# Kernel tuning notes

Measured on AMD Instinct MI355X. Metric: run time of the kernel, lower is better.

Reference implementation:

```python
import jax, jax.numpy as jnp
import numpy as np

D_MODEL = 1024
N_HEADS = 16
DK = D_MODEL // N_HEADS


def setup_inputs() -> dict:
    key = jax.random.key(0)
    k1, k2, k3, k4 = jax.random.split(key, 4)
    x = jax.random.normal(k1, (2, 2048, D_MODEL), dtype=jnp.float32)
    # torch nn.Linear stores weight as [out_features, in_features]
    W_qkv = jax.random.normal(k2, (3 * D_MODEL, D_MODEL), dtype=jnp.float32) * (1.0 / np.sqrt(D_MODEL))
    W_proj = jax.random.normal(k3, (D_MODEL, D_MODEL), dtype=jnp.float32) * (1.0 / np.sqrt(D_MODEL))
    b_proj = jax.random.normal(k4, (D_MODEL,), dtype=jnp.float32) * 0.01
    return {"x": x, "W_qkv": W_qkv, "W_proj": W_proj, "b_proj": b_proj}


def reference(x, W_qkv, W_proj, b_proj):
    B, L, D = x.shape
    qkv = x @ W_qkv.T                      # [B, L, 3D]
    q, k, v = jnp.split(qkv, 3, axis=-1)   # each [B, L, D]

    def split_heads(t):
        return t.reshape(B, L, N_HEADS, DK).transpose(0, 2, 1, 3)  # [B, H, L, dk]

    q, k, v = map(split_heads, (q, k, v))
    scale = jnp.float32(1.0 / np.sqrt(DK))
    scores = jnp.einsum('bhid,bhjd->bhij', q, k) * scale  # [B, H, L, L]
    attn = jax.nn.softmax(scores, axis=-1)
    out = jnp.einsum('bhij,bhjd->bhid', attn, v)           # [B, H, L, dk]
    out = out.transpose(0, 2, 1, 3).reshape(B, L, D)
    return out @ W_proj.T + b_proj
```

## Files before the change

kernel.cpp:

```cpp
#include <hip/hip_runtime.h>
#include <stdint.h>

typedef unsigned short ushort_t;
typedef __bf16 bf16x4 __attribute__((ext_vector_type(4)));
typedef __bf16 bf16x8 __attribute__((ext_vector_type(8)));
typedef float f32x4 __attribute__((ext_vector_type(4)));
typedef float f32x16 __attribute__((ext_vector_type(16)));
typedef unsigned short us8 __attribute__((ext_vector_type(8)));
typedef unsigned short us4v __attribute__((ext_vector_type(4)));

__device__ __forceinline__ float bf2f(ushort_t u) {
  union { uint32_t u; float f; } v; v.u = ((uint32_t)u) << 16; return v.f;
}
__device__ __forceinline__ ushort_t f2bf(float f) {
  union { float f; uint32_t u; } v; v.f = f;
  uint32_t u = v.u;
  uint32_t r = (u + 0x7FFFu + ((u >> 16) & 1u)) >> 16;
  return (ushort_t)r;
}
__device__ __forceinline__ uint32_t pkbf(float a, float b) {
  __bf16 x = (__bf16)a, y = (__bf16)b;
  uint32_t ux = __builtin_bit_cast(unsigned short, x);
  uint32_t uy = __builtin_bit_cast(unsigned short, y);
  return ux | (uy << 16);
}
__device__ __forceinline__ void gload_lds16(const void* g, void* l) {
  __builtin_amdgcn_global_load_lds(
      (const __attribute__((address_space(1))) void*)g,
      (__attribute__((address_space(3))) void*)l, 16, 0, 0);
}
__device__ __forceinline__ void tr2(const ushort_t* p, bf16x4& lo, bf16x4& hi) {
  asm volatile("ds_read_b64_tr_b16 %0, %2\n\t"
               "ds_read_b64_tr_b16 %1, %2 offset:128"
               : "=&v"(lo), "=&v"(hi)
               : "v"((const __attribute__((address_space(3))) ushort_t*)p));
}

template <typename T> __device__ __forceinline__ T to_out(float f);
template <> __device__ __forceinline__ ushort_t to_out<ushort_t>(float f) { return f2bf(f); }
template <> __device__ __forceinline__ float to_out<float>(float f) { return f; }

#define SCQ 0.1803368801111204f

__global__ void f2b3_kernel(const float* __restrict__ a, ushort_t* __restrict__ ao,
                            const float* __restrict__ b, ushort_t* __restrict__ bo,
                            const float* __restrict__ c, ushort_t* __restrict__ co) {
  int blk = blockIdx.x;
  const float* src; ushort_t* dst; int n4, b0, nb;
  if (blk < 1024)      { src = a; dst = ao; n4 = 1048576; b0 = blk;        nb = 1024; }
  else if (blk < 1792) { src = b; dst = bo; n4 = 786432;  b0 = blk - 1024; nb = 768; }
  else                 { src = c; dst = co; n4 = 262144;  b0 = blk - 1792; nb = 256; }
  for (int i = b0 * 256 + threadIdx.x; i < n4; i += nb * 256) {
    float4 v = ((const float4*)src)[i];
    us4v o;
    o[0] = f2bf(v.x); o[1] = f2bf(v.y); o[2] = f2bf(v.z); o[3] = f2bf(v.w);
    ((us4v*)dst)[i] = o;
  }
}

template<bool BIAS, typename OT, bool SCALEQ>
__global__ __launch_bounds__(256, 2) void gemm_bt(
    const ushort_t* __restrict__ A, const ushort_t* __restrict__ W,
    const float* __restrict__ bias, OT* __restrict__ C,
    int M, int N, int K)
{
  __shared__ ushort_t As[128 * 64];
  __shared__ ushort_t Bs[128 * 64];
  const int t = threadIdx.x;
  const int w = t >> 6, lane = t & 63;
  const int lg = lane >> 4, lc = lane & 15;

  const int NX = N >> 7;
  const int nwg = gridDim.x;
  const int o = blockIdx.x;
  const int id = (o & 7) * (nwg >> 3) + (o >> 3);
  const int rowbase = (id / NX) * 128;
  const int colbase = (id % NX) * 128;
  const int wr = (w >> 1) * 64, wc = (w & 1) * 64;

  f32x4 acc[4][4] = {};
  const int nkt = K >> 6;

  for (int kt = 0; kt < nkt; ++kt) {
#pragma unroll
    for (int i = 0; i < 4; ++i) {
      int off = (i * 256 + t) * 16;
      int row = off >> 7;
      int cb  = off & 127;
      int ec  = cb ^ ((row & 7) << 4);
      gload_lds16(A + (size_t)(rowbase + row) * K + kt * 64 + (ec >> 1),
                  (char*)As + off);
      gload_lds16(W + (size_t)(colbase + row) * K + kt * 64 + (ec >> 1),
                  (char*)Bs + off);
    }
    __syncthreads();
#pragma unroll
    for (int kk = 0; kk < 2; ++kk) {
      bf16x8 af[4], bf[4];
#pragma unroll
      for (int m = 0; m < 4; ++m) {
        int row = wr + m * 16 + lc;
        int kb  = (lg * 16 + kk * 64) ^ ((row & 7) << 4);
        af[m] = *(const bf16x8*)((const char*)As + row * 128 + kb);
        int col = wc + m * 16 + lc;
        int kb2 = (lg * 16 + kk * 64) ^ ((col & 7) << 4);
        bf[m] = *(const bf16x8*)((const char*)Bs + col * 128 + kb2);
      }
#pragma unroll
      for (int m = 0; m < 4; ++m)
#pragma unroll
        for (int n = 0; n < 4; ++n)
          acc[m][n] = __builtin_amdgcn_mfma_f32_16x16x32_bf16(af[m], bf[n],
                                                              acc[m][n], 0, 0, 0);
    }
    __syncthreads();
  }

#pragma unroll
  for (int m = 0; m < 4; ++m) {
    int r0 = rowbase + wr + m * 16 + lg * 4;
#pragma unroll
    for (int n = 0; n < 4; ++n) {
      int c0 = colbase + wc + n * 16 + lc;
      float bv = 0.f;
      if (BIAS) bv = bias[c0];
      float qs = 1.f;
      if (SCALEQ) qs = (c0 < 1024) ? SCQ : 1.f;
#pragma unroll
      for (int j = 0; j < 4; ++j)
        C[(size_t)(r0 + j) * N + c0] = to_out<OT>(acc[m][n][j] * qs + bv);
    }
  }
}

__global__ __launch_bounds__(512, 4) void attn_fwd(
    const ushort_t* __restrict__ qkv, ushort_t* __restrict__ o1,
    ushort_t* __restrict__ o2, float* __restrict__ lbuf)
{
  __shared__ ushort_t Ks[2][64 * 64];
  __shared__ ushort_t Vs[2][64 * 64];

  const int t = threadIdx.x, w = t >> 6, lane = t & 63;
  const int l31 = lane & 31, hi = lane >> 5;
  const int lc = lane & 15;

  const int d = blockIdx.x;
  const int qt = (d >> 3) & 7;
  const int bhs = (d & 7) * 8 + (d >> 6);
  const int bh = bhs >> 1, split = bhs & 1;
  const int b = bh >> 4, h = bh & 15;

  const ushort_t* Qg = qkv + (size_t)(b * 2048) * 3072 + h * 64;
  const ushort_t* Kg = Qg + 1024 + (size_t)split * 1024 * 3072;
  const ushort_t* Vg = Qg + 2048 + (size_t)split * 1024 * 3072;

  auto stage_k = [&](ushort_t* Kd, int kt) {
    int off = t * 16;
    int row = off >> 7;
    int cb  = off & 127;
    int ec  = cb ^ ((row & 7) << 4);
    gload_lds16(Kg + (size_t)(kt * 64 + row) * 3072 + (ec >> 1),
                (char*)Kd + off);
  };
  const int vr  = t >> 3;
  const int vc0 = (t & 7) * 8;
  const int vdst = (vc0 >> 4) * 2048 + (vr >> 2) * 128 + (vr & 3) * 32 +
                   (vc0 & 8) * 2;

  const ushort_t* qrow_p = Qg + (size_t)(qt * 256 + w * 32 + l31) * 3072;
  bf16x8 qf[4];
#pragma unroll
  for (int kk = 0; kk < 4; ++kk)
    qf[kk] = *(const bf16x8*)(qrow_p + kk * 16 + hi * 8);

  stage_k(Ks[0], 0);
  {
    us8 v = *(const us8*)(Vg + (size_t)vr * 3072 + vc0);
    *(us8*)((char*)Vs[0] + vdst) = v;
  }
  __syncthreads();

  f32x16 oacc0 = {}, oacc1 = {};
  float l = 0.f;
  const int m16 = (lane >> 4) & 1;

  int cur = 0;
  for (int kt = 0; kt < 16; ++kt) {
    us8 vnext;
    if (kt < 15) {
      stage_k(Ks[cur ^ 1], kt + 1);
      vnext = *(const us8*)(Vg + (size_t)((kt + 1) * 64 + vr) * 3072 + vc0);
    }

    const ushort_t* Kc = Ks[cur];
    f32x16 s0 = {}, s1 = {};
    __builtin_amdgcn_s_setprio(1);
#pragma unroll
    for (int kk = 0; kk < 4; ++kk) {
      int cbyte = (kk * 32 + hi * 16);
      int r0 = l31, r1 = 32 + l31;
      bf16x8 kf0 = *(const bf16x8*)((const char*)Kc + r0 * 128 +
                                    (cbyte ^ ((r0 & 7) << 4)));
      bf16x8 kf1 = *(const bf16x8*)((const char*)Kc + r1 * 128 +
                                    (cbyte ^ ((r1 & 7) << 4)));
      s0 = __builtin_amdgcn_mfma_f32_32x32x16_bf16(kf0, qf[kk], s0, 0, 0, 0);
      s1 = __builtin_amdgcn_mfma_f32_32x32x16_bf16(kf1, qf[kk], s1, 0, 0, 0);
    }
    __builtin_amdgcn_s_setprio(0);

#pragma unroll
    for (int i = 0; i < 16; ++i) {
      s0[i] = __builtin_amdgcn_exp2f(s0[i]);
      s1[i] = __builtin_amdgcn_exp2f(s1[i]);
    }
    float rs = (((s0[0] + s0[1]) + (s0[2] + s0[3])) +
                ((s0[4] + s0[5]) + (s0[6] + s0[7]))) +
               (((s0[8] + s0[9]) + (s0[10] + s0[11])) +
                ((s0[12] + s0[13]) + (s0[14] + s0[15])));
    float rt = (((s1[0] + s1[1]) + (s1[2] + s1[3])) +
                ((s1[4] + s1[5]) + (s1[6] + s1[7]))) +
               (((s1[8] + s1[9]) + (s1[10] + s1[11])) +
                ((s1[12] + s1[13]) + (s1[14] + s1[15])));
    l += rs + rt;

    uint32_t pk0[8], pk1[8];
#pragma unroll
    for (int j = 0; j < 8; ++j) {
      pk0[j] = pkbf(s0[2 * j], s0[2 * j + 1]);
      pk1[j] = pkbf(s1[2 * j], s1[2 * j + 1]);
    }

    if (kt < 15)
      *(us8*)((char*)Vs[cur ^ 1] + vdst) = vnext;

    const ushort_t* Vc = Vs[cur];
    bf16x8 pa[4], vf[4][2];
#pragma unroll
    for (int ks = 0; ks < 4; ++ks) {
      int j0 = 4 * (ks & 1);
      uint32_t x0 = (ks < 2) ? pk0[j0]     : pk1[j0];
      uint32_t x1 = (ks < 2) ? pk0[j0 + 1] : pk1[j0 + 1];
      uint32_t y0 = (ks < 2) ? pk0[j0 + 2] : pk1[j0 + 2];
      uint32_t y1 = (ks < 2) ? pk0[j0 + 3] : pk1[j0 + 3];
      asm volatile("v_permlane32_swap_b32 %0, %1" : "+v"(x0), "+v"(y0));
      asm volatile("v_permlane32_swap_b32 %0, %1" : "+v"(x1), "+v"(y1));
      union { uint32_t du[4]; bf16x8 v; } U;
      U.du[0] = x0; U.du[1] = x1; U.du[2] = y0; U.du[3] = y1;
      pa[ks] = U.v;
#pragma unroll
      for (int nd = 0; nd < 2; ++nd) {
        bf16x4 lo, hh;
        tr2(Vc + (nd * 2 + m16) * 1024 + (4 * ks + 2 * hi) * 64 + lc * 4, lo, hh);
        vf[ks][nd] = __builtin_shufflevector(lo, hh, 0, 1, 2, 3, 4, 5, 6, 7);
      }
    }
    asm volatile("s_waitcnt lgkmcnt(0)" ::: "memory");
    __builtin_amdgcn_sched_barrier(0);
    __builtin_amdgcn_s_setprio(1);
#pragma unroll
    for (int ks = 0; ks < 4; ++ks) {
      oacc0 = __builtin_amdgcn_mfma_f32_32x32x16_bf16(pa[ks], vf[ks][0], oacc0, 0, 0, 0);
      oacc1 = __builtin_amdgcn_mfma_f32_32x32x16_bf16(pa[ks], vf[ks][1], oacc1, 0, 0, 0);
    }
    __builtin_amdgcn_s_setprio(0);

    __syncthreads();
    cur ^= 1;
  }

  l += __shfl_xor(l, 32);

  ushort_t* op = split ? o2 : o1;
#pragma unroll
  for (int r = 0; r < 16; ++r) {
    int crow = (r & 3) + 8 * (r >> 2) + 4 * hi;
    int qrow = qt * 256 + w * 32 + crow;
    size_t base = ((size_t)(b * 2048 + qrow)) * 1024 + h * 64 + l31;
    op[base]      = f2bf(oacc0[r]);
    op[base + 32] = f2bf(oacc1[r]);
  }
  if (hi == 0) {
    int qrow = qt * 256 + w * 32 + l31;
    lbuf[(size_t)split * 65536 + (size_t)(b * 2048 + qrow) * 16 + h] = l;
  }
}

__global__ void merge_kernel(ushort_t* __restrict__ o1,
                             const ushort_t* __restrict__ o2,
                             const float* __restrict__ lbuf) {
  int i = blockIdx.x * blockDim.x + threadIdx.x;
  int row = i >> 7;
  int col = (i & 127) * 8;
  int h = col >> 6;
  float l1 = lbuf[(size_t)row * 16 + h];
  float l2 = lbuf[65536 + (size_t)row * 16 + h];
  float inv = 1.f / (l1 + l2);
  us8 v1 = ((const us8*)o1)[i];
  us8 v2 = ((const us8*)o2)[i];
  us8 o;
#pragma unroll
  for (int j = 0; j < 8; ++j)
    o[j] = f2bf((bf2f(v1[j]) + bf2f(v2[j])) * inv);
  ((us8*)o1)[i] = o;
}

extern "C" void kernel_launch(void* const* d_in, const int* in_sizes, int n_in,
                              void* d_out, int out_size, void* d_ws, size_t ws_size,
                              hipStream_t stream) {
  const float* x     = (const float*)d_in[0];
  const float* Wqkv  = (const float*)d_in[1];
  const float* Wproj = (const float*)d_in[2];
  const float* bproj = (const float*)d_in[3];
  float* out = (float*)d_out;

  ushort_t* qkv   = (ushort_t*)d_ws;
  ushort_t* o1    = qkv   + (size_t)4096 * 3072;
  ushort_t* xb    = o1    + (size_t)4096 * 1024;
  ushort_t* wqb   = xb    + (size_t)4096 * 1024;
  ushort_t* wpb   = wqb   + (size_t)3072 * 1024;
  float*    lbuf  = (float*)(wpb + (size_t)1024 * 1024);

  dim3 blk(256);
  f2b3_kernel<<<2048, blk, 0, stream>>>(x, xb, Wqkv, wqb, Wproj, wpb);

  gemm_bt<false, ushort_t, true><<<768, blk, 0, stream>>>(
      xb, wqb, nullptr, qkv, 4096, 3072, 1024);
  attn_fwd<<<dim3(512), dim3(512), 0, stream>>>(qkv, o1, xb, lbuf);
  merge_kernel<<<2048, blk, 0, stream>>>(o1, xb, lbuf);
  gemm_bt<true, float, false><<<256, blk, 0, stream>>>(
      o1, wpb, bproj, out, 4096, 1024, 1024);
}
```

Before: 111.1 us.

## Fuse split-KV merge into attention kernel via atomic completion flags

```diff
diff --git a/kernel.cpp b/kernel.cpp
--- a/kernel.cpp
+++ b/kernel.cpp
@@ -44,12 +44,14 @@
 
 __global__ void f2b3_kernel(const float* __restrict__ a, ushort_t* __restrict__ ao,
                             const float* __restrict__ b, ushort_t* __restrict__ bo,
-                            const float* __restrict__ c, ushort_t* __restrict__ co) {
+                            const float* __restrict__ c, ushort_t* __restrict__ co,
+                            int* __restrict__ flags) {
   int blk = blockIdx.x;
   const float* src; ushort_t* dst; int n4, b0, nb;
   if (blk < 1024)      { src = a; dst = ao; n4 = 1048576; b0 = blk;        nb = 1024; }
   else if (blk < 1792) { src = b; dst = bo; n4 = 786432;  b0 = blk - 1024; nb = 768; }
-  else                 { src = c; dst = co; n4 = 262144;  b0 = blk - 1792; nb = 256; }
+  else                 { src = c; dst = co; n4 = 262144;  b0 = blk - 1792; nb = 256;
+                         if (threadIdx.x == 0) flags[blk - 1792] = 0; }
   for (int i = b0 * 256 + threadIdx.x; i < n4; i += nb * 256) {
     float4 v = ((const float4*)src)[i];
     us4v o;
@@ -135,7 +137,8 @@
 
 __global__ __launch_bounds__(512, 4) void attn_fwd(
     const ushort_t* __restrict__ qkv, ushort_t* __restrict__ o1,
-    ushort_t* __restrict__ o2, float* __restrict__ lbuf)
+    ushort_t* __restrict__ o2, float* __restrict__ lbuf,
+    int* __restrict__ flags)
 {
   __shared__ ushort_t Ks[2][64 * 64];
   __shared__ ushort_t Vs[2][64 * 64];
@@ -271,37 +274,37 @@
   l += __shfl_xor(l, 32);
 
   ushort_t* op = split ? o2 : o1;
+  const int qrow0 = qt * 256 + w * 32;
 #pragma unroll
   for (int r = 0; r < 16; ++r) {
     int crow = (r & 3) + 8 * (r >> 2) + 4 * hi;
-    int qrow = qt * 256 + w * 32 + crow;
-    size_t base = ((size_t)(b * 2048 + qrow)) * 1024 + h * 64 + l31;
+    size_t base = ((size_t)(b * 2048 + qrow0 + crow)) * 1024 + h * 64 + l31;
     op[base]      = f2bf(oacc0[r]);
     op[base + 32] = f2bf(oacc1[r]);
   }
-  if (hi == 0) {
-    int qrow = qt * 256 + w * 32 + l31;
-    lbuf[(size_t)split * 65536 + (size_t)(b * 2048 + qrow) * 16 + h] = l;
-  }
-}
-
-__global__ void merge_kernel(ushort_t* __restrict__ o1,
-                             const ushort_t* __restrict__ o2,
-                             const float* __restrict__ lbuf) {
-  int i = blockIdx.x * blockDim.x + threadIdx.x;
-  int row = i >> 7;
-  int col = (i & 127) * 8;
-  int h = col >> 6;
-  float l1 = lbuf[(size_t)row * 16 + h];
-  float l2 = lbuf[65536 + (size_t)row * 16 + h];
-  float inv = 1.f / (l1 + l2);
-  us8 v1 = ((const us8*)o1)[i];
-  us8 v2 = ((const us8*)o2)[i];
-  us8 o;
-#pragma unroll
-  for (int j = 0; j < 8; ++j)
-    o[j] = f2bf((bf2f(v1[j]) + bf2f(v2[j])) * inv);
-  ((us8*)o1)[i] = o;
+  if (hi == 0)
+    lbuf[(size_t)split * 65536 + (size_t)(b * 2048 + qrow0 + l31) * 16 + h] = l;
+
+  __threadfence();
+  __syncthreads();
+  __shared__ int s_old;
+  if (t == 0) s_old = atomicAdd(&flags[bh * 8 + qt], 1);
+  __syncthreads();
+  if (s_old == 1) {
+    __threadfence();
+    const ushort_t* other = split ? o1 : o2;
+    float lo = lbuf[(size_t)(split ^ 1) * 65536 +
+                    (size_t)(b * 2048 + qrow0 + l31) * 16 + h];
+    float linv = 1.f / (l + lo);
+#pragma unroll
+    for (int r = 0; r < 16; ++r) {
+      int crow = (r & 3) + 8 * (r >> 2) + 4 * hi;
+      float iq = __shfl(linv, crow);
+      size_t base = ((size_t)(b * 2048 + qrow0 + crow)) * 1024 + h * 64 + l31;
+      o1[base]      = f2bf((bf2f(f2bf(oacc0[r])) + bf2f(other[base])) * iq);
+      o1[base + 32] = f2bf((bf2f(f2bf(oacc1[r])) + bf2f(other[base + 32])) * iq);
+    }
+  }
 }
 
 extern "C" void kernel_launch(void* const* d_in, const int* in_sizes, int n_in,
@@ -319,14 +322,14 @@
   ushort_t* wqb   = xb    + (size_t)4096 * 1024;
   ushort_t* wpb   = wqb   + (size_t)3072 * 1024;
   float*    lbuf  = (float*)(wpb + (size_t)1024 * 1024);
+  int*      flags = (int*)(lbuf + (size_t)2 * 65536);
 
   dim3 blk(256);
-  f2b3_kernel<<<2048, blk, 0, stream>>>(x, xb, Wqkv, wqb, Wproj, wpb);
+  f2b3_kernel<<<2048, blk, 0, stream>>>(x, xb, Wqkv, wqb, Wproj, wpb, flags);
 
   gemm_bt<false, ushort_t, true><<<768, blk, 0, stream>>>(
       xb, wqb, nullptr, qkv, 4096, 3072, 1024);
-  attn_fwd<<<dim3(512), dim3(512), 0, stream>>>(qkv, o1, xb, lbuf);
-  merge_kernel<<<2048, blk, 0, stream>>>(o1, xb, lbuf);
+  attn_fwd<<<dim3(512), dim3(512), 0, stream>>>(qkv, o1, xb, lbuf, flags);
   gemm_bt<true, float, false><<<256, blk, 0, stream>>>(
       o1, wpb, bproj, out, 4096, 1024, 1024);
 }
```

Measured after the change: 287.6 us. 159% more time.
